# Performance work log

Measured on AMD Instinct MI355X. Metric: run time of the kernel, lower is better.

## Reference

```python
import jax, jax.numpy as jnp
import numpy as np
import math

D_MODEL = 1024
NUM_HEADS = 16
D_K = D_MODEL // NUM_HEADS
B, S = 2, 2048


def setup_inputs() -> dict:
    key = jax.random.key(0)
    ks = jax.random.split(key, 11)
    scale = 1.0 / math.sqrt(D_MODEL)
    inp = {
        "query": jax.random.normal(ks[0], (B, S, D_MODEL), jnp.float32),
        "key": jax.random.normal(ks[1], (B, S, D_MODEL), jnp.float32),
        "value": jax.random.normal(ks[2], (B, S, D_MODEL), jnp.float32),
        "Wq": jax.random.normal(ks[3], (D_MODEL, D_MODEL), jnp.float32) * scale,
        "bq": jnp.zeros((D_MODEL,), jnp.float32),
        "Wk": jax.random.normal(ks[4], (D_MODEL, D_MODEL), jnp.float32) * scale,
        "bk": jnp.zeros((D_MODEL,), jnp.float32),
        "Wv": jax.random.normal(ks[5], (D_MODEL, D_MODEL), jnp.float32) * scale,
        "bv": jnp.zeros((D_MODEL,), jnp.float32),
        "Wo": jax.random.normal(ks[6], (D_MODEL, D_MODEL), jnp.float32) * scale,
        "bo": jnp.zeros((D_MODEL,), jnp.float32),
    }
    return inp


def reference(query, key, value, Wq, bq, Wk, bk, Wv, bv, Wo, bo):
    b, s, _ = query.shape
    # QKV projections (torch Linear: x @ W.T + b)
    Q = query @ Wq.T + bq
    K = key @ Wk.T + bk
    V = value @ Wv.T + bv
    # [b, h, s, d_k]
    Q = Q.reshape(b, s, NUM_HEADS, D_K).transpose(0, 2, 1, 3)
    K = K.reshape(b, s, NUM_HEADS, D_K).transpose(0, 2, 1, 3)
    V = V.reshape(b, s, NUM_HEADS, D_K).transpose(0, 2, 1, 3)
    score = jnp.einsum("bhqd,bhkd->bhqk", Q, K) / math.sqrt(D_K)
    attn = jax.nn.softmax(score, axis=-1)
    out = jnp.einsum("bhqk,bhkd->bhqd", attn, V)
    out = out.transpose(0, 2, 1, 3).reshape(b, s, D_MODEL)
    return out @ Wo.T + bo
```

## Files before the change

### kernel.cpp

```cpp
#include <hip/hip_runtime.h>

#define NHEADS 16
#define SEQ    2048
#define BATCH  2
#define DMODEL 1024
#define MTOT   4096

typedef __attribute__((ext_vector_type(8)))  short short8;
typedef __attribute__((ext_vector_type(4)))  float f32x4;
typedef __attribute__((ext_vector_type(16))) float f32x16;

__device__ __forceinline__ unsigned short f32_to_bf16_rn(float x) {
  unsigned int u = __float_as_uint(x);
  u += 0x7fffu + ((u >> 16) & 1u);
  return (unsigned short)(u >> 16);
}

__device__ __forceinline__ unsigned cvt_pk_bf16(float lo, float hi_) {
  unsigned r;
  asm("v_cvt_pk_bf16_f32 %0, %1, %2" : "=v"(r) : "v"(lo), "v"(hi_));
  return r;
}

__device__ __forceinline__ void permlane32_swap(unsigned &a, unsigned &b) {
  asm("v_permlane32_swap_b32 %0, %1" : "+v"(a), "+v"(b));
}

__device__ __forceinline__ void async16(void* lds, const void* g) {
  __builtin_amdgcn_global_load_lds((const __attribute__((address_space(1))) unsigned int*)g,
                                   (__attribute__((address_space(3))) unsigned int*)lds, 16, 0, 0);
}

__global__ void cvt_bf16_kernel(const float* __restrict__ x0, const float* __restrict__ x1,
                                const float* __restrict__ x2,
                                const float* __restrict__ w0, const float* __restrict__ w1,
                                const float* __restrict__ w2, const float* __restrict__ w3,
                                unsigned short* __restrict__ obase)
{
  const int e = (blockIdx.x*256 + threadIdx.x)*8;
  const float* src;
  int local;
  if (e < 3*4194304) {
    const int t = e >> 22;
    src = t==0 ? x0 : t==1 ? x1 : x2;
    local = e & (4194304-1);
    src += local;
    local += t << 22;
  } else {
    const int f = e - 3*4194304;
    const int t = f >> 20;
    src = t==0 ? w0 : t==1 ? w1 : t==2 ? w2 : w3;
    src += (f & (1048576-1));
    local = e;
  }
  const float4 v0 = *(const float4*)(src);
  const float4 v1 = *(const float4*)(src + 4);
  union { unsigned short u[8]; uint4 v; } r;
  r.u[0] = f32_to_bf16_rn(v0.x); r.u[1] = f32_to_bf16_rn(v0.y);
  r.u[2] = f32_to_bf16_rn(v0.z); r.u[3] = f32_to_bf16_rn(v0.w);
  r.u[4] = f32_to_bf16_rn(v1.x); r.u[5] = f32_to_bf16_rn(v1.y);
  r.u[6] = f32_to_bf16_rn(v1.z); r.u[7] = f32_to_bf16_rn(v1.w);
  *(uint4*)(obase + local) = r.v;
}

template<int BM>
__device__ __forceinline__ void gemm_core(const unsigned short* __restrict__ A,
                                          const unsigned short* __restrict__ W,
                                          unsigned short* sA, unsigned short* sB,
                                          int m0, int n0, f32x4 (&acc)[BM/32][4])
{
  constexpr int MI = BM/32;
  const int t = threadIdx.x;
  const int lane = t & 63;
  const int wv = t >> 6;
  const int wm = wv >> 1, wn = wv & 1;
  const int lr = lane & 15, lk = lane >> 4;

  for (int kt = 0; kt < DMODEL/64; ++kt) {
    #pragma unroll
    for (int g = 0; g < MI; ++g) {
      const int o  = g*4096 + t*16;
      const int so = o ^ (((o >> 7) & 7) << 4);
      const int row = so >> 7, colE = (so & 127) >> 1;
      async16((char*)sA + o, A + (size_t)(m0 + row)*DMODEL + kt*64 + colE);
    }
    #pragma unroll
    for (int g = 0; g < 4; ++g) {
      const int o  = g*4096 + t*16;
      const int so = o ^ (((o >> 7) & 7) << 4);
      const int row = so >> 7, colE = (so & 127) >> 1;
      async16((char*)sB + o, W + (size_t)(n0 + row)*DMODEL + kt*64 + colE);
    }
    __syncthreads();
    #pragma unroll
    for (int ks = 0; ks < 2; ++ks) {
      short8 af[MI], bf[4];
      #pragma unroll
      for (int mi = 0; mi < MI; ++mi) {
        const int row = wm*(BM/2) + mi*16 + lr;
        const int sl  = (ks*4 + lk) ^ (row & 7);
        af[mi] = *(const short8*)(sA + row*64 + sl*8);
      }
      #pragma unroll
      for (int ni = 0; ni < 4; ++ni) {
        const int row = wn*64 + ni*16 + lr;
        const int sl  = (ks*4 + lk) ^ (row & 7);
        bf[ni] = *(const short8*)(sB + row*64 + sl*8);
      }
      #pragma unroll
      for (int mi = 0; mi < MI; ++mi)
        #pragma unroll
        for (int ni = 0; ni < 4; ++ni)
          acc[mi][ni] = __builtin_amdgcn_mfma_f32_16x16x32_bf16(af[mi], bf[ni], acc[mi][ni], 0, 0, 0);
    }
    __syncthreads();
  }
}

__global__ __launch_bounds__(256, 3)
void qkv_gemm_kernel(const unsigned short* __restrict__ Xq, const unsigned short* __restrict__ Xk,
                     const unsigned short* __restrict__ Xv,
                     const unsigned short* __restrict__ Wq, const unsigned short* __restrict__ Wk,
                     const unsigned short* __restrict__ Wv,
                     const float* __restrict__ bq, const float* __restrict__ bk,
                     const float* __restrict__ bv,
                     unsigned short* __restrict__ Qp, unsigned short* __restrict__ Kp,
                     unsigned short* __restrict__ Vtp)
{
  constexpr int BM = 128;
  constexpr int MI = BM/32;
  __shared__ __align__(16) unsigned short smem[17024];
  unsigned short* sA = smem;
  unsigned short* sB = smem + 8192;

  const int m0   = blockIdx.x * BM;
  const int nabs = blockIdx.y * 128;
  const int wsel = nabs >> 10;
  const int n0   = nabs & 1023;
  const unsigned short* A = wsel==0 ? Xq : wsel==1 ? Xk : Xv;
  const unsigned short* W = wsel==0 ? Wq : wsel==1 ? Wk : Wv;
  const float* bias       = wsel==0 ? bq : wsel==1 ? bk : bv;

  f32x4 acc[MI][4];
  #pragma unroll
  for (int mi = 0; mi < MI; ++mi)
    #pragma unroll
    for (int ni = 0; ni < 4; ++ni)
      acc[mi][ni] = {0.f, 0.f, 0.f, 0.f};

  gemm_core<BM>(A, W, sA, sB, m0, n0, acc);

  const int t = threadIdx.x, lane = t & 63, wvx = t >> 6;
  const int wm = wvx >> 1, wn = wvx & 1;
  const int lr = lane & 15, lk = lane >> 4;

  if (wsel == 2) {
    #pragma unroll
    for (int ni = 0; ni < 4; ++ni) {
      const float badd = bias[n0 + wn*64 + ni*16 + lr];
      #pragma unroll
      for (int mi = 0; mi < MI; ++mi)
        #pragma unroll
        for (int r = 0; r < 4; ++r) {
          const int ml = wm*(BM/2) + mi*16 + lk*4 + r;
          smem[(wn*64 + ni*16 + lr)*132 + ml] = f32_to_bf16_rn(acc[mi][ni][r] + badd);
        }
    }
    __syncthreads();
    const int bb = m0 >> 11, s0 = m0 & 2047;
    const int jr = (t & 15)*8, nr = t >> 4;
    #pragma unroll
    for (int pass = 0; pass < 8; ++pass) {
      const int n  = pass*16 + nr;
      const int nn = n0 + n, hh = nn >> 6, d = nn & 63;
      const short8 v = *(const short8*)(smem + n*132 + jr);
      *(short8*)(Vtp + (((size_t)bb*NHEADS + hh)*64 + d)*SEQ + s0 + jr) = v;
    }
  } else {
    unsigned short* dst = wsel==0 ? Qp : Kp;
    const float qscale = (wsel == 0) ? 0.125f * 1.4426950408889634f : 1.0f;
    #pragma unroll
    for (int ni = 0; ni < 4; ++ni) {
      const int nn = n0 + wn*64 + ni*16 + lr;
      const float badd = bias[nn];
      const int hh = nn >> 6, d = nn & 63;
      #pragma unroll
      for (int mi = 0; mi < MI; ++mi) {
        #pragma unroll
        for (int r = 0; r < 4; ++r) {
          const int m = m0 + wm*(BM/2) + mi*16 + lk*4 + r;
          const int bb = m >> 11, s = m & 2047;
          const float v = (acc[mi][ni][r] + badd) * qscale;
          dst[(((size_t)bb*NHEADS + hh)*SEQ + s)*64 + d] = f32_to_bf16_rn(v);
        }
      }
    }
  }
}

__global__ __launch_bounds__(256, 2)
void attn_kernel(const unsigned short* __restrict__ Qp, const unsigned short* __restrict__ Kp,
                 const unsigned short* __restrict__ Vtp, unsigned short* __restrict__ Op)
{
  __shared__ __align__(16) unsigned short sm[16384];
  constexpr int NT = SEQ/64;

  const int t = threadIdx.x, lane = t & 63, w = t >> 6;
  const int lq = lane & 31, hi = lane >> 5;
  const int f   = blockIdx.x;
  const int wid = (f & 7)*64 + (f >> 3);
  const int qt = wid & 15, h = (wid >> 4) & 15, b = wid >> 8;

  const size_t bh = (size_t)b*NHEADS + h;
  const unsigned short* Qh = Qp  + bh*SEQ*64;
  const unsigned short* Kh = Kp  + bh*SEQ*64;
  const unsigned short* Vh = Vtp + bh*64*SEQ;
  const int q0 = qt*128 + w*32;

  short8 qf[4];
  #pragma unroll
  for (int ks = 0; ks < 4; ++ks)
    qf[ks] = *(const short8*)(Qh + (size_t)(q0 + lq)*64 + ks*16 + hi*8);

  f32x16 z16;
  #pragma unroll
  for (int r = 0; r < 16; ++r) z16[r] = 0.f;

  const unsigned short* srcp0;
  size_t sstride;
  if (w < 2) { srcp0 = Kh + (size_t)(w*32 + lq)*64 + hi*8;       sstride = 64*64; }
  else       { srcp0 = Vh + (size_t)((w-2)*32 + lq)*2048 + hi*8; sstride = 64;    }

  #pragma unroll
  for (int i = 0; i < 4; ++i)
    async16((char*)sm + w*4096 + i*1024, srcp0 + i*16);

  f32x16 o[2];
  float lsa[4] = {0.f, 0.f, 0.f, 0.f};
  #pragma unroll
  for (int d = 0; d < 2; ++d)
    #pragma unroll
    for (int r = 0; r < 16; ++r) o[d][r] = 0.f;

  for (int kt = 0; kt < NT; ++kt) {
    {
      const unsigned short* sp = srcp0 + (size_t)((kt + 1) & (NT - 1))*sstride;
      const int nb = ((kt + 1) & 1) * 16384;
      #pragma unroll
      for (int i = 0; i < 4; ++i)
        async16((char*)sm + nb + w*4096 + i*1024, sp + i*16);
    }
    asm volatile("s_waitcnt vmcnt(4)" ::: "memory");
    __builtin_amdgcn_s_barrier();

    const unsigned short* base  = sm + (kt & 1)*8192;
    const unsigned short* vbase = base + 4096;

    f32x16 st[2];
    #pragma unroll
    for (int sub = 0; sub < 2; ++sub) {
      #pragma unroll
      for (int ks = 0; ks < 4; ++ks) {
        const short8 kf = *(const short8*)(base + (sub*4 + ks)*512 + lane*8);
        if (ks == 0)
          st[sub] = __builtin_amdgcn_mfma_f32_32x32x16_bf16(kf, qf[0], z16, 0, 0, 0);
        else
          st[sub] = __builtin_amdgcn_mfma_f32_32x32x16_bf16(kf, qf[ks], st[sub], 0, 0, 0);
      }
    }

    unsigned pw[2][8];
    #pragma unroll
    for (int sub = 0; sub < 2; ++sub) {
      #pragma unroll
      for (int r = 0; r < 16; ++r) {
        const float p = __builtin_amdgcn_exp2f(st[sub][r]);
        st[sub][r] = p;
        lsa[r & 3] += p;
      }
      unsigned x0 = cvt_pk_bf16(st[sub][0],  st[sub][1]);
      unsigned x1 = cvt_pk_bf16(st[sub][2],  st[sub][3]);
      unsigned y0 = cvt_pk_bf16(st[sub][4],  st[sub][5]);
      unsigned y1 = cvt_pk_bf16(st[sub][6],  st[sub][7]);
      permlane32_swap(x0, y0);
      permlane32_swap(x1, y1);
      pw[sub][0] = x0; pw[sub][1] = x1; pw[sub][2] = y0; pw[sub][3] = y1;
      unsigned z0 = cvt_pk_bf16(st[sub][8],  st[sub][9]);
      unsigned z1 = cvt_pk_bf16(st[sub][10], st[sub][11]);
      unsigned w0 = cvt_pk_bf16(st[sub][12], st[sub][13]);
      unsigned w1 = cvt_pk_bf16(st[sub][14], st[sub][15]);
      permlane32_swap(z0, w0);
      permlane32_swap(z1, w1);
      pw[sub][4] = z0; pw[sub][5] = z1; pw[sub][6] = w0; pw[sub][7] = w1;
    }

    #pragma unroll
    for (int sub = 0; sub < 2; ++sub) {
      const short8 v00 = *(const short8*)(vbase + (0*4 + 2*sub    )*512 + lane*8);
      const short8 v01 = *(const short8*)(vbase + (0*4 + 2*sub + 1)*512 + lane*8);
      const short8 v10 = *(const short8*)(vbase + (1*4 + 2*sub    )*512 + lane*8);
      const short8 v11 = *(const short8*)(vbase + (1*4 + 2*sub + 1)*512 + lane*8);
      union { unsigned u[4]; short8 s; } pA, pB;
      pA.u[0] = pw[sub][0]; pA.u[1] = pw[sub][1]; pA.u[2] = pw[sub][2]; pA.u[3] = pw[sub][3];
      pB.u[0] = pw[sub][4]; pB.u[1] = pw[sub][5]; pB.u[2] = pw[sub][6]; pB.u[3] = pw[sub][7];
      o[0] = __builtin_amdgcn_mfma_f32_32x32x16_bf16(v00, pA.s, o[0], 0, 0, 0);
      o[1] = __builtin_amdgcn_mfma_f32_32x32x16_bf16(v10, pA.s, o[1], 0, 0, 0);
      o[0] = __builtin_amdgcn_mfma_f32_32x32x16_bf16(v01, pB.s, o[0], 0, 0, 0);
      o[1] = __builtin_amdgcn_mfma_f32_32x32x16_bf16(v11, pB.s, o[1], 0, 0, 0);
    }
    asm volatile("" ::: "memory");
    __builtin_amdgcn_s_barrier();
  }

  float lsum = (lsa[0] + lsa[1]) + (lsa[2] + lsa[3]);
  lsum += __shfl_xor(lsum, 32);
  const float inv = __builtin_amdgcn_rcpf(lsum);
  unsigned short* orow = Op + ((size_t)b*SEQ + q0 + lq)*DMODEL + h*64;
  #pragma unroll
  for (int dblk = 0; dblk < 2; ++dblk)
    #pragma unroll
    for (int g = 0; g < 4; ++g) {
      union { unsigned short us[4]; uint2 v; } pk;
      #pragma unroll
      for (int r = 0; r < 4; ++r) pk.us[r] = f32_to_bf16_rn(o[dblk][g*4 + r] * inv);
      *(uint2*)(orow + dblk*32 + g*8 + hi*4) = pk.v;
    }
}

__global__ __launch_bounds__(256, 2)
void oproj_gemm_kernel(const unsigned short* __restrict__ Oin, const unsigned short* __restrict__ Wo,
                       const float* __restrict__ bo, float* __restrict__ out)
{
  constexpr int BM = 64;
  constexpr int MI = BM/32;
  __shared__ __align__(16) unsigned short sA[BM*64];
  __shared__ __align__(16) unsigned short sB[128*64];
  const int m0 = blockIdx.x * BM;
  const int n0 = blockIdx.y * 128;

  f32x4 acc[MI][4];
  #pragma unroll
  for (int mi = 0; mi < MI; ++mi)
    #pragma unroll
    for (int ni = 0; ni < 4; ++ni)
      acc[mi][ni] = {0.f,0.f,0.f,0.f};

  gemm_core<BM>(Oin, Wo, sA, sB, m0, n0, acc);

  const int t = threadIdx.x, lane = t & 63, wvx = t >> 6;
  const int wm = wvx >> 1, wn = wvx & 1;
  const int lr = lane & 15, lk = lane >> 4;

  #pragma unroll
  for (int ni = 0; ni < 4; ++ni) {
    const int nn = n0 + wn*64 + ni*16 + lr;
    const float badd = bo[nn];
    #pragma unroll
    for (int mi = 0; mi < MI; ++mi)
      #pragma unroll
      for (int r = 0; r < 4; ++r) {
        const int m = m0 + wm*(BM/2) + mi*16 + lk*4 + r;
        out[(size_t)m*DMODEL + nn] = acc[mi][ni][r] + badd;
      }
  }
}

extern "C" void kernel_launch(void* const* d_in, const int* in_sizes, int n_in,
                              void* d_out, int out_size, void* d_ws, size_t ws_size,
                              hipStream_t stream) {
  const float* query = (const float*)d_in[0];
  const float* key   = (const float*)d_in[1];
  const float* value = (const float*)d_in[2];
  const float* Wq    = (const float*)d_in[3];
  const float* bq    = (const float*)d_in[4];
  const float* Wk    = (const float*)d_in[5];
  const float* bk    = (const float*)d_in[6];
  const float* Wv    = (const float*)d_in[7];
  const float* bv    = (const float*)d_in[8];
  const float* Wo    = (const float*)d_in[9];
  const float* bo    = (const float*)d_in[10];

  const size_t NX = (size_t)MTOT*DMODEL;
  const size_t NW = (size_t)DMODEL*DMODEL;
  unsigned short* w   = (unsigned short*)d_ws;
  unsigned short* Xq  = w;
  unsigned short* Xk  = Xq  + NX;
  unsigned short* Xv  = Xk  + NX;
  unsigned short* Wqp = Xv  + NX;
  unsigned short* Wkp = Wqp + NW;
  unsigned short* Wvp = Wkp + NW;
  unsigned short* Wop = Wvp + NW;
  unsigned short* Qp  = Wop + NW;
  unsigned short* Kp  = Qp  + NX;
  unsigned short* Vtp = Kp  + NX;
  unsigned short* Opb = Vtp + NX;

  cvt_bf16_kernel<<<dim3(8192), 256, 0, stream>>>(
      query, key, value, Wq, Wk, Wv, Wo, w);
  qkv_gemm_kernel<<<dim3(32, 24), 256, 0, stream>>>(
      Xq, Xk, Xv, Wqp, Wkp, Wvp, bq, bk, bv, Qp, Kp, Vtp);
  attn_kernel<<<dim3(512), 256, 0, stream>>>(Qp, Kp, Vtp, Opb);
  oproj_gemm_kernel<<<dim3(64, 8), 256, 0, stream>>>(Opb, Wop, bo, (float*)d_out);
}
```

Measured before the change: 109.9 us.

## Fuse fp32-to-bf16 activation conversion into QKV GEMM with register-staged A loads

Removes the separate conversion pass over the three fp32 activation tensors. The QKV GEMM now loads fp32 A tiles into registers, converts them with packed bf16 instructions, and writes them swizzled into LDS. The B (weight) tiles are double-buffered via async global-to-LDS loads that overlap with the MFMA work. This saves a full write-and-read round trip of the bf16 activations, but each GEMM block now reads the fp32 A data, twice the bytes, once per N-tile, and uses more LDS, which may lower occupancy.

```diff
diff --git a/kernel.cpp b/kernel.cpp
--- a/kernel.cpp
+++ b/kernel.cpp
@@ -31,36 +31,21 @@
                                    (__attribute__((address_space(3))) unsigned int*)lds, 16, 0, 0);
 }
 
-__global__ void cvt_bf16_kernel(const float* __restrict__ x0, const float* __restrict__ x1,
-                                const float* __restrict__ x2,
-                                const float* __restrict__ w0, const float* __restrict__ w1,
-                                const float* __restrict__ w2, const float* __restrict__ w3,
-                                unsigned short* __restrict__ obase)
+__global__ void cvt_w_kernel(const float* __restrict__ w0, const float* __restrict__ w1,
+                             const float* __restrict__ w2, const float* __restrict__ w3,
+                             unsigned short* __restrict__ obase)
 {
-  const int e = (blockIdx.x*256 + threadIdx.x)*8;
-  const float* src;
-  int local;
-  if (e < 3*4194304) {
-    const int t = e >> 22;
-    src = t==0 ? x0 : t==1 ? x1 : x2;
-    local = e & (4194304-1);
-    src += local;
-    local += t << 22;
-  } else {
-    const int f = e - 3*4194304;
-    const int t = f >> 20;
-    src = t==0 ? w0 : t==1 ? w1 : t==2 ? w2 : w3;
-    src += (f & (1048576-1));
-    local = e;
-  }
-  const float4 v0 = *(const float4*)(src);
-  const float4 v1 = *(const float4*)(src + 4);
+  const int which = blockIdx.y;
+  const float* src = which==0 ? w0 : which==1 ? w1 : which==2 ? w2 : w3;
+  const int i = (blockIdx.x*256 + threadIdx.x)*8;
+  const float4 v0 = *(const float4*)(src + i);
+  const float4 v1 = *(const float4*)(src + i + 4);
   union { unsigned short u[8]; uint4 v; } r;
   r.u[0] = f32_to_bf16_rn(v0.x); r.u[1] = f32_to_bf16_rn(v0.y);
   r.u[2] = f32_to_bf16_rn(v0.z); r.u[3] = f32_to_bf16_rn(v0.w);
   r.u[4] = f32_to_bf16_rn(v1.x); r.u[5] = f32_to_bf16_rn(v1.y);
   r.u[6] = f32_to_bf16_rn(v1.z); r.u[7] = f32_to_bf16_rn(v1.w);
-  *(uint4*)(obase + local) = r.v;
+  *(uint4*)(obase + (size_t)which*1048576 + i) = r.v;
 }
 
 template<int BM>
@@ -118,8 +103,8 @@
 }
 
 __global__ __launch_bounds__(256, 3)
-void qkv_gemm_kernel(const unsigned short* __restrict__ Xq, const unsigned short* __restrict__ Xk,
-                     const unsigned short* __restrict__ Xv,
+void qkv_gemm_kernel(const float* __restrict__ Xq, const float* __restrict__ Xk,
+                     const float* __restrict__ Xv,
                      const unsigned short* __restrict__ Wq, const unsigned short* __restrict__ Wk,
                      const unsigned short* __restrict__ Wv,
                      const float* __restrict__ bq, const float* __restrict__ bk,
@@ -127,33 +112,100 @@
                      unsigned short* __restrict__ Qp, unsigned short* __restrict__ Kp,
                      unsigned short* __restrict__ Vtp)
 {
-  constexpr int BM = 128;
-  constexpr int MI = BM/32;
-  __shared__ __align__(16) unsigned short smem[17024];
+  constexpr int MI = 4;
+  constexpr int NK = DMODEL/64;
+  __shared__ __align__(16) unsigned short smem[24576];
   unsigned short* sA = smem;
-  unsigned short* sB = smem + 8192;
-
-  const int m0   = blockIdx.x * BM;
+
+  const int m0   = blockIdx.x * 128;
   const int nabs = blockIdx.y * 128;
   const int wsel = nabs >> 10;
   const int n0   = nabs & 1023;
-  const unsigned short* A = wsel==0 ? Xq : wsel==1 ? Xk : Xv;
+  const float* A          = wsel==0 ? Xq : wsel==1 ? Xk : Xv;
   const unsigned short* W = wsel==0 ? Wq : wsel==1 ? Wk : Wv;
   const float* bias       = wsel==0 ? bq : wsel==1 ? bk : bv;
-
-  f32x4 acc[MI][4];
-  #pragma unroll
-  for (int mi = 0; mi < MI; ++mi)
-    #pragma unroll
-    for (int ni = 0; ni < 4; ++ni)
-      acc[mi][ni] = {0.f, 0.f, 0.f, 0.f};
-
-  gemm_core<BM>(A, W, sA, sB, m0, n0, acc);
 
   const int t = threadIdx.x, lane = t & 63, wvx = t >> 6;
   const int wm = wvx >> 1, wn = wvx & 1;
   const int lr = lane & 15, lk = lane >> 4;
 
+  int aRow[MI], aCol[MI], aO[MI];
+  #pragma unroll
+  for (int g = 0; g < MI; ++g) {
+    const int o  = g*4096 + t*16;
+    const int so = o ^ (((o >> 7) & 7) << 4);
+    aO[g] = o; aRow[g] = so >> 7; aCol[g] = (so & 127) >> 1;
+  }
+
+  f32x4 acc[MI][4];
+  #pragma unroll
+  for (int mi = 0; mi < MI; ++mi)
+    #pragma unroll
+    for (int ni = 0; ni < 4; ++ni)
+      acc[mi][ni] = {0.f, 0.f, 0.f, 0.f};
+
+  float4 aLo[MI], aHi[MI];
+  #pragma unroll
+  for (int g = 0; g < MI; ++g) {
+    const float* s = A + (size_t)(m0 + aRow[g])*DMODEL + aCol[g];
+    aLo[g] = *(const float4*)(s);
+    aHi[g] = *(const float4*)(s + 4);
+  }
+  #pragma unroll
+  for (int g = 0; g < 4; ++g)
+    async16((char*)smem + 16384 + aO[g], W + (size_t)(n0 + aRow[g])*DMODEL + aCol[g]);
+
+  for (int kt = 0; kt < NK; ++kt) {
+    asm volatile("s_waitcnt vmcnt(0)" ::: "memory");
+    #pragma unroll
+    for (int g = 0; g < MI; ++g) {
+      union { uint4 v; unsigned u[4]; } r;
+      r.u[0] = cvt_pk_bf16(aLo[g].x, aLo[g].y);
+      r.u[1] = cvt_pk_bf16(aLo[g].z, aLo[g].w);
+      r.u[2] = cvt_pk_bf16(aHi[g].x, aHi[g].y);
+      r.u[3] = cvt_pk_bf16(aHi[g].z, aHi[g].w);
+      *(uint4*)((char*)sA + aO[g]) = r.v;
+    }
+    asm volatile("s_waitcnt lgkmcnt(0)" ::: "memory");
+    __builtin_amdgcn_s_barrier();
+    if (kt + 1 < NK) {
+      #pragma unroll
+      for (int g = 0; g < MI; ++g) {
+        const float* s = A + (size_t)(m0 + aRow[g])*DMODEL + (kt + 1)*64 + aCol[g];
+        aLo[g] = *(const float4*)(s);
+        aHi[g] = *(const float4*)(s + 4);
+      }
+      const int nb = 16384 + ((kt + 1) & 1)*8192*2;
+      #pragma unroll
+      for (int g = 0; g < 4; ++g)
+        async16((char*)smem + nb + aO[g], W + (size_t)(n0 + aRow[g])*DMODEL + (kt + 1)*64 + aCol[g]);
+    }
+    const unsigned short* sB = smem + 8192 + (kt & 1)*8192;
+    #pragma unroll
+    for (int ks = 0; ks < 2; ++ks) {
+      short8 af[MI], bf[4];
+      #pragma unroll
+      for (int mi = 0; mi < MI; ++mi) {
+        const int row = wm*64 + mi*16 + lr;
+        const int sl  = (ks*4 + lk) ^ (row & 7);
+        af[mi] = *(const short8*)(sA + row*64 + sl*8);
+      }
+      #pragma unroll
+      for (int ni = 0; ni < 4; ++ni) {
+        const int row = wn*64 + ni*16 + lr;
+        const int sl  = (ks*4 + lk) ^ (row & 7);
+        bf[ni] = *(const short8*)(sB + row*64 + sl*8);
+      }
+      #pragma unroll
+      for (int mi = 0; mi < MI; ++mi)
+        #pragma unroll
+        for (int ni = 0; ni < 4; ++ni)
+          acc[mi][ni] = __builtin_amdgcn_mfma_f32_16x16x32_bf16(af[mi], bf[ni], acc[mi][ni], 0, 0, 0);
+    }
+    __builtin_amdgcn_s_barrier();
+  }
+  __syncthreads();
+
   if (wsel == 2) {
     #pragma unroll
     for (int ni = 0; ni < 4; ++ni) {
@@ -162,7 +214,7 @@
       for (int mi = 0; mi < MI; ++mi)
         #pragma unroll
         for (int r = 0; r < 4; ++r) {
-          const int ml = wm*(BM/2) + mi*16 + lk*4 + r;
+          const int ml = wm*64 + mi*16 + lk*4 + r;
           smem[(wn*64 + ni*16 + lr)*132 + ml] = f32_to_bf16_rn(acc[mi][ni][r] + badd);
         }
     }
@@ -188,7 +240,7 @@
       for (int mi = 0; mi < MI; ++mi) {
         #pragma unroll
         for (int r = 0; r < 4; ++r) {
-          const int m = m0 + wm*(BM/2) + mi*16 + lk*4 + r;
+          const int m = m0 + wm*64 + mi*16 + lk*4 + r;
           const int bb = m >> 11, s = m & 2047;
           const float v = (acc[mi][ni][r] + badd) * qscale;
           dst[(((size_t)bb*NHEADS + hh)*SEQ + s)*64 + d] = f32_to_bf16_rn(v);
@@ -383,10 +435,7 @@
   const size_t NX = (size_t)MTOT*DMODEL;
   const size_t NW = (size_t)DMODEL*DMODEL;
   unsigned short* w   = (unsigned short*)d_ws;
-  unsigned short* Xq  = w;
-  unsigned short* Xk  = Xq  + NX;
-  unsigned short* Xv  = Xk  + NX;
-  unsigned short* Wqp = Xv  + NX;
+  unsigned short* Wqp = w + 3*NX;
   unsigned short* Wkp = Wqp + NW;
   unsigned short* Wvp = Wkp + NW;
   unsigned short* Wop = Wvp + NW;
@@ -395,10 +444,9 @@
   unsigned short* Vtp = Kp  + NX;
   unsigned short* Opb = Vtp + NX;
 
-  cvt_bf16_kernel<<<dim3(8192), 256, 0, stream>>>(
-      query, key, value, Wq, Wk, Wv, Wo, w);
+  cvt_w_kernel<<<dim3(512, 4), 256, 0, stream>>>(Wq, Wk, Wv, Wo, Wqp);
   qkv_gemm_kernel<<<dim3(32, 24), 256, 0, stream>>>(
-      Xq, Xk, Xv, Wqp, Wkp, Wvp, bq, bk, bv, Qp, Kp, Vtp);
+      query, key, value, Wqp, Wkp, Wvp, bq, bk, bv, Qp, Kp, Vtp);
   attn_kernel<<<dim3(512), 256, 0, stream>>>(Qp, Kp, Vtp, Opb);
   oproj_gemm_kernel<<<dim3(64, 8), 256, 0, stream>>>(Opb, Wop, bo, (float*)d_out);
 }
```

After: 105.0 us, median of 3. 4.5% less time.
